# Performance work log

Measured on AMD Instinct MI355X. Metric: run time of the kernel, lower is better.

The kernel has to match this reference:

```python
import jax, jax.numpy as jnp
import numpy as np

N_AGENTS, OBS_DIM, HID, ACT_DIM = 8192, 64, 128, 16


def setup_inputs() -> dict:
    key = jax.random.key(0)
    k = jax.random.split(key, 8)
    obs_agents = jax.random.normal(k[0], (N_AGENTS, OBS_DIM), dtype=jnp.float32)
    # binary adjacency, {0,1}, int32 (index/mask semantics, non-differentiable)
    adj = jax.random.randint(k[1], (N_AGENTS, N_AGENTS), 0, 2, dtype=jnp.int32)
    def lin(kk, fan_in, fan_out):
        lim = 1.0 / np.sqrt(fan_in)
        kw, kb = jax.random.split(kk)
        W = jax.random.uniform(kw, (fan_in, fan_out), jnp.float32, -lim, lim)
        b = jax.random.uniform(kb, (fan_out,), jnp.float32, -lim, lim)
        return W, b
    W1, b1 = lin(k[2], OBS_DIM, HID)          # encoder
    W2, b2 = lin(k[3], 2 * HID, HID)          # actor layer 1
    W3, b3 = lin(k[4], HID, ACT_DIM)          # actor layer 2
    return {"obs_agents": obs_agents, "adj": adj,
            "W1": W1, "b1": b1, "W2": W2, "b2": b2, "W3": W3, "b3": b3}


def reference(obs_agents, adj, W1, b1, W2, b2, W3, b3):
    # per-agent encode: h = tanh(obs @ W1 + b1)  -> [N, HID]
    h = jnp.tanh(obs_agents @ W1 + b1)
    # neighbor mean message: mean of h[j] over j with adj[i,j]!=0, zeros if no neighbors
    a = adj.astype(h.dtype)                      # [N, N] binary
    deg = jnp.sum(a, axis=1, keepdims=True)      # [N, 1]
    msg = (a @ h) / jnp.maximum(deg, 1.0)        # zero rows stay zero
    # actor MLP on concat([h, msg])
    combined = jnp.concatenate([h, msg], axis=-1)            # [N, 2*HID]
    hid = jnp.tanh(combined @ W2 + b2)                        # [N, HID]
    logits = hid @ W3 + b3                                    # [N, ACT_DIM]
    return logits
```

## Files before the change

### kernel.cpp

```cpp
#include <hip/hip_runtime.h>
#include <stdint.h>
#include <math.h>

#define NAG 8192
#define NC  128
#define NSPLIT 8
#define LDB2 136

typedef __attribute__((ext_vector_type(8))) short short8;
typedef __attribute__((ext_vector_type(4))) float floatx4;

__device__ __forceinline__ float bf2f(unsigned short u) {
    union { uint32_t i; float f; } v; v.i = ((uint32_t)u) << 16; return v.f;
}
__device__ __forceinline__ unsigned short f2bf(float f) {
    union { float f; uint32_t i; } v; v.f = f;
    uint32_t x = v.i;
    return (unsigned short)((x + 0x7FFFu + ((x >> 16) & 1u)) >> 16);
}
__device__ __forceinline__ unsigned short f2h(float f) {
    union { _Float16 h; unsigned short u; } v; v.h = (_Float16)f; return v.u;
}
__device__ __forceinline__ float h2f(unsigned short u) {
    union { _Float16 h; unsigned short u; } v; v.u = u; return (float)v.h;
}
__device__ __forceinline__ bool detect_f32(const void* W1, int t) {
    const unsigned short* w = (const unsigned short*)W1;
    int l = t & 63, big = 0;
    #pragma unroll
    for (int j = 0; j < 8; ++j) {
        float v = bf2f(w[l * 8 + j]);
        if (!(fabsf(v) <= 1e6f)) big = 1;
    }
    return __ballot(big) != 0ull;
}

__global__ __launch_bounds__(256) void kE_encode(
    const void* __restrict__ obs,
    const void* __restrict__ W1,
    const void* __restrict__ b1,
    float* __restrict__ h_f32,
    unsigned short* __restrict__ hT)
{
    __shared__ float obs_lds[32][68];
    __shared__ unsigned short ht_lds[128][33];
    const int t = threadIdx.x;
    const int abase = blockIdx.x * 32;
    const bool isf = detect_f32(W1, t);

    {
        int a = t >> 3, c0 = (t & 7) * 8;
        if (isf) {
            const float* p = (const float*)obs;
            #pragma unroll
            for (int j = 0; j < 8; ++j)
                obs_lds[a][c0 + j] = p[(size_t)(abase + a) * 64 + c0 + j];
        } else {
            const unsigned short* p = (const unsigned short*)obs;
            #pragma unroll
            for (int j = 0; j < 8; ++j)
                obs_lds[a][c0 + j] = bf2f(p[(size_t)(abase + a) * 64 + c0 + j]);
        }
    }
    __syncthreads();

    const int o = t & 127;
    const int half = t >> 7;
    float acc[16];
    if (isf) {
        const float* Wp = (const float*)W1;
        float bias = ((const float*)b1)[o];
        #pragma unroll
        for (int i = 0; i < 16; ++i) acc[i] = bias;
        for (int k0 = 0; k0 < 64; k0 += 8) {
            float w[8];
            #pragma unroll
            for (int j = 0; j < 8; ++j) w[j] = Wp[(k0 + j) * 128 + o];
            #pragma unroll
            for (int j = 0; j < 8; ++j)
                #pragma unroll
                for (int i = 0; i < 16; ++i)
                    acc[i] = fmaf(obs_lds[half * 16 + i][k0 + j], w[j], acc[i]);
        }
    } else {
        const unsigned short* Wp = (const unsigned short*)W1;
        float bias = bf2f(((const unsigned short*)b1)[o]);
        #pragma unroll
        for (int i = 0; i < 16; ++i) acc[i] = bias;
        for (int k0 = 0; k0 < 64; k0 += 8) {
            float w[8];
            #pragma unroll
            for (int j = 0; j < 8; ++j) w[j] = bf2f(Wp[(k0 + j) * 128 + o]);
            #pragma unroll
            for (int j = 0; j < 8; ++j)
                #pragma unroll
                for (int i = 0; i < 16; ++i)
                    acc[i] = fmaf(obs_lds[half * 16 + i][k0 + j], w[j], acc[i]);
        }
    }
    #pragma unroll
    for (int i = 0; i < 16; ++i) {
        float th = tanhf(acc[i]);
        int a = half * 16 + i;
        h_f32[(size_t)(abase + a) * 128 + o] = th;
        ht_lds[o][a] = f2bf(th);
    }
    __syncthreads();

    for (int p = 0; p < 16; ++p) {
        int n = p * 8 + (t >> 5);
        int a = t & 31;
        hT[(size_t)n * NAG + abase + a] = ht_lds[n][a];
    }
}

__global__ __launch_bounds__(256, 4) void kG_msggemm(
    const int* __restrict__ adj,
    const unsigned short* __restrict__ hT,
    unsigned short* __restrict__ Cp16,
    int* __restrict__ degP)
{
    __shared__ __align__(16) unsigned short Blds[128 * LDB2];
    const int t = threadIdx.x;
    const int mtile = blockIdx.x & 127;
    const int ks = blockIdx.x >> 7;
    const int row0 = mtile * 64;
    const int kbeg = ks * 1024;

    const int wave = t >> 6, lane = t & 63;
    const int fm = lane & 15, quad = lane >> 4;

    floatx4 acc[8];
    #pragma unroll
    for (int i = 0; i < 8; ++i) acc[i] = (floatx4)0.f;

    const int arow = row0 + wave * 16 + fm;
    const int* ap = adj + (size_t)arow * NAG + kbeg + quad * 8;
    int dsum = 0;

    for (int ss = 0; ss < 8; ++ss) {
        int4 av[8];
        #pragma unroll
        for (int kw = 0; kw < 4; ++kw) {
            av[2 * kw]     = *reinterpret_cast<const int4*>(ap + ss * 128 + kw * 32);
            av[2 * kw + 1] = *reinterpret_cast<const int4*>(ap + ss * 128 + kw * 32 + 4);
        }
        if (ss) __syncthreads();
        #pragma unroll
        for (int i = 0; i < 8; ++i) {
            int idx = i * 256 + t;
            int row = idx >> 4, ch = idx & 15;
            uint4 v = *reinterpret_cast<const uint4*>(hT + (size_t)row * NAG + kbeg + ss * 128 + ch * 8);
            *reinterpret_cast<uint4*>(&Blds[row * LDB2 + ch * 8]) = v;
        }
        __syncthreads();
        #pragma unroll
        for (int kw = 0; kw < 4; ++kw) {
            const int* q = (const int*)&av[2 * kw];
            union { uint32_t u[4]; short8 s; } af;
            #pragma unroll
            for (int p = 0; p < 4; ++p) {
                uint32_t e0 = (q[2 * p]     != 0);
                uint32_t e1 = (q[2 * p + 1] != 0);
                dsum += (int)(e0 + e1);
                af.u[p] = (e0 | (e1 << 16)) * 0x3F80u;
            }
            #pragma unroll
            for (int j = 0; j < 8; ++j) {
                short8 bf = *reinterpret_cast<const short8*>(&Blds[(j * 16 + fm) * LDB2 + kw * 32 + quad * 8]);
                acc[j] = __builtin_amdgcn_mfma_f32_16x16x32_bf16(af.s, bf, acc[j], 0, 0, 0);
            }
        }
    }

    dsum += __shfl_xor(dsum, 16);
    dsum += __shfl_xor(dsum, 32);
    if (lane < 16) degP[ks * NAG + arow] = dsum;

    unsigned short* out = Cp16 + (size_t)ks * (NAG * NC);
    #pragma unroll
    for (int j = 0; j < 8; ++j) {
        int col = j * 16 + fm;
        #pragma unroll
        for (int r = 0; r < 4; ++r) {
            int row = row0 + wave * 16 + quad * 4 + r;
            out[(size_t)row * NC + col] = f2h(acc[j][r]);
        }
    }
}

__global__ __launch_bounds__(256) void k3_actor(
    const float* __restrict__ h_f32,
    const unsigned short* __restrict__ Cp16,
    const int* __restrict__ degP,
    const void* __restrict__ W1,
    const void* __restrict__ W2,
    const void* __restrict__ b2,
    const void* __restrict__ W3,
    const void* __restrict__ b3,
    void* __restrict__ out)
{
    __shared__ float4 comb4[8][66];
    __shared__ float hid[8][132];
    __shared__ int degs[8][9];
    __shared__ float inv_lds[8];
    const int t = threadIdx.x;
    const int abase = blockIdx.x * 8;
    const bool isf = detect_f32(W1, t);
    const size_t PS = (size_t)NAG * NC;

    if (t < 64) {
        int a = t >> 3, s = t & 7;
        degs[a][s] = degP[s * NAG + abase + a];
    }
    __syncthreads();
    if (t < 8) {
        int d = 0;
        #pragma unroll
        for (int s = 0; s < 8; ++s) d += degs[t][s];
        inv_lds[t] = 1.0f / fmaxf((float)d, 1.0f);
    }
    __syncthreads();

    #pragma unroll
    for (int jj = 0; jj < 2; ++jj) {
        int idx = jj * 256 + t;
        int a = idx >> 6, q = idx & 63;
        float4 v;
        if (q < 32) {
            v = *reinterpret_cast<const float4*>(h_f32 + (size_t)(abase + a) * 128 + q * 4);
        } else {
            int f = (q - 32) * 4;
            float s0 = 0.f, s1 = 0.f, s2 = 0.f, s3 = 0.f;
            #pragma unroll
            for (int s = 0; s < NSPLIT; ++s) {
                ushort4 p = *reinterpret_cast<const ushort4*>(Cp16 + s * PS + (size_t)(abase + a) * NC + f);
                s0 += h2f(p.x); s1 += h2f(p.y); s2 += h2f(p.z); s3 += h2f(p.w);
            }
            float sc = inv_lds[a];
            v = make_float4(s0 * sc, s1 * sc, s2 * sc, s3 * sc);
        }
        comb4[a][q] = v;
    }
    __syncthreads();

    const int o = t & 127, half = t >> 7;
    float acc[4];
    if (isf) {
        const float* Wp = (const float*)W2;
        float bias = ((const float*)b2)[o];
        #pragma unroll
        for (int i = 0; i < 4; ++i) acc[i] = bias;
        for (int cq = 0; cq < 64; ++cq) {
            float w0 = Wp[(cq * 4 + 0) * 128 + o];
            float w1 = Wp[(cq * 4 + 1) * 128 + o];
            float w2 = Wp[(cq * 4 + 2) * 128 + o];
            float w3 = Wp[(cq * 4 + 3) * 128 + o];
            #pragma unroll
            for (int i = 0; i < 4; ++i) {
                float4 v = comb4[half * 4 + i][cq];
                acc[i] = fmaf(v.x, w0, acc[i]);
                acc[i] = fmaf(v.y, w1, acc[i]);
                acc[i] = fmaf(v.z, w2, acc[i]);
                acc[i] = fmaf(v.w, w3, acc[i]);
            }
        }
    } else {
        const unsigned short* Wp = (const unsigned short*)W2;
        float bias = bf2f(((const unsigned short*)b2)[o]);
        #pragma unroll
        for (int i = 0; i < 4; ++i) acc[i] = bias;
        for (int cq = 0; cq < 64; ++cq) {
            float w0 = bf2f(Wp[(cq * 4 + 0) * 128 + o]);
            float w1 = bf2f(Wp[(cq * 4 + 1) * 128 + o]);
            float w2 = bf2f(Wp[(cq * 4 + 2) * 128 + o]);
            float w3 = bf2f(Wp[(cq * 4 + 3) * 128 + o]);
            #pragma unroll
            for (int i = 0; i < 4; ++i) {
                float4 v = comb4[half * 4 + i][cq];
                acc[i] = fmaf(v.x, w0, acc[i]);
                acc[i] = fmaf(v.y, w1, acc[i]);
                acc[i] = fmaf(v.z, w2, acc[i]);
                acc[i] = fmaf(v.w, w3, acc[i]);
            }
        }
    }
    #pragma unroll
    for (int i = 0; i < 4; ++i)
        hid[half * 4 + i][o] = tanhf(acc[i]);
    __syncthreads();

    if (t < 128) {
        const int q = t & 15, ar = t >> 4;
        float l;
        if (isf) {
            const float* Wp = (const float*)W3;
            l = ((const float*)b3)[q];
            #pragma unroll 4
            for (int oo = 0; oo < 128; ++oo)
                l = fmaf(hid[ar][oo], Wp[oo * 16 + q], l);
        } else {
            const unsigned short* Wp = (const unsigned short*)W3;
            l = bf2f(((const unsigned short*)b3)[q]);
            #pragma unroll 4
            for (int oo = 0; oo < 128; ++oo)
                l = fmaf(hid[ar][oo], bf2f(Wp[oo * 16 + q]), l);
        }
        size_t i0 = (size_t)(abase + ar) * 16 + q;
        if (isf) ((float*)out)[i0] = l;
        else     ((unsigned short*)out)[i0] = f2bf(l);
    }
}

extern "C" void kernel_launch(void* const* d_in, const int* in_sizes, int n_in,
                              void* d_out, int out_size, void* d_ws, size_t ws_size,
                              hipStream_t stream) {
    const void* obs = d_in[0];
    const int*  adj = (const int*)d_in[1];
    const void* W1  = d_in[2];
    const void* b1  = d_in[3];
    const void* W2  = d_in[4];
    const void* b2  = d_in[5];
    const void* W3  = d_in[6];
    const void* b3  = d_in[7];

    char* ws = (char*)d_ws;
    unsigned short* hT   = (unsigned short*)(ws);
    float*          h_f32= (float*)(ws + 2097152);
    unsigned short* Cp16 = (unsigned short*)(ws + 6291456);
    int*            degP = (int*)(ws + 23068672);

    hipLaunchKernelGGL(kE_encode, dim3(256), dim3(256), 0, stream,
                       obs, W1, b1, h_f32, hT);
    hipLaunchKernelGGL(kG_msggemm, dim3(1024), dim3(256), 0, stream,
                       adj, hT, Cp16, degP);
    hipLaunchKernelGGL(k3_actor, dim3(1024), dim3(256), 0, stream,
                       h_f32, Cp16, degP, W1, W2, b2, W3, b3, d_out);
}
```

Measured before the change: 484.2 us.

## Load adjacency rows coalesced and pack into bitmasks via ballot

The adjacency tile is now read with lanes spanning consecutive columns of one row, so each load is a fully coalesced 256-byte access instead of each lane pulling 32-byte strided chunks from its own row. Each wave ballots the nonzero flags into 64-bit masks, stores them in a small LDS array, and every lane then rebuilds its MFMA A fragment and the degree count from those bits with popcount. This removes the per-element compare work from the fragment path and the degree shuffle reduction. It costs 32 scalar loads per stage instead of 8 vector loads, plus ballot and LDS traffic.

```diff
diff --git a/kernel.cpp b/kernel.cpp
--- a/kernel.cpp
+++ b/kernel.cpp
@@ -121,6 +121,7 @@
     int* __restrict__ degP)
 {
     __shared__ __align__(16) unsigned short Blds[128 * LDB2];
+    __shared__ __align__(16) unsigned long long bitsLds[4][16][2];
     const int t = threadIdx.x;
     const int mtile = blockIdx.x & 127;
     const int ks = blockIdx.x >> 7;
@@ -135,15 +136,15 @@
     for (int i = 0; i < 8; ++i) acc[i] = (floatx4)0.f;
 
     const int arow = row0 + wave * 16 + fm;
-    const int* ap = adj + (size_t)arow * NAG + kbeg + quad * 8;
+    const int* wrows = adj + (size_t)(row0 + wave * 16) * NAG + kbeg;
     int dsum = 0;
 
     for (int ss = 0; ss < 8; ++ss) {
-        int4 av[8];
-        #pragma unroll
-        for (int kw = 0; kw < 4; ++kw) {
-            av[2 * kw]     = *reinterpret_cast<const int4*>(ap + ss * 128 + kw * 32);
-            av[2 * kw + 1] = *reinterpret_cast<const int4*>(ap + ss * 128 + kw * 32 + 4);
+        int va[32];
+        #pragma unroll
+        for (int i = 0; i < 32; ++i) {
+            int r = i >> 1, hh = i & 1;
+            va[i] = wrows[(size_t)r * NAG + ss * 128 + hh * 64 + lane];
         }
         if (ss) __syncthreads();
         #pragma unroll
@@ -153,17 +154,23 @@
             uint4 v = *reinterpret_cast<const uint4*>(hT + (size_t)row * NAG + kbeg + ss * 128 + ch * 8);
             *reinterpret_cast<uint4*>(&Blds[row * LDB2 + ch * 8]) = v;
         }
+        #pragma unroll
+        for (int i = 0; i < 32; ++i) {
+            unsigned long long m = __ballot(va[i] != 0);
+            if (lane == 0) bitsLds[wave][i >> 1][i & 1] = m;
+        }
         __syncthreads();
+        int4 a0 = *reinterpret_cast<const int4*>(&bitsLds[wave][fm][0]);
+        uint32_t aw[4] = {(uint32_t)a0.x, (uint32_t)a0.y, (uint32_t)a0.z, (uint32_t)a0.w};
+        dsum += __popc(aw[0]) + __popc(aw[1]) + __popc(aw[2]) + __popc(aw[3]);
         #pragma unroll
         for (int kw = 0; kw < 4; ++kw) {
-            const int* q = (const int*)&av[2 * kw];
+            uint32_t b = (aw[kw] >> (quad * 8)) & 0xFFu;
             union { uint32_t u[4]; short8 s; } af;
             #pragma unroll
             for (int p = 0; p < 4; ++p) {
-                uint32_t e0 = (q[2 * p]     != 0);
-                uint32_t e1 = (q[2 * p + 1] != 0);
-                dsum += (int)(e0 + e1);
-                af.u[p] = (e0 | (e1 << 16)) * 0x3F80u;
+                uint32_t bb = b >> (2 * p);
+                af.u[p] = ((bb & 1u) | ((bb & 2u) << 15)) * 0x3F80u;
             }
             #pragma unroll
             for (int j = 0; j < 8; ++j) {
@@ -173,9 +180,7 @@
         }
     }
 
-    dsum += __shfl_xor(dsum, 16);
-    dsum += __shfl_xor(dsum, 32);
-    if (lane < 16) degP[ks * NAG + arow] = dsum;
+    if (quad == 0) degP[ks * NAG + arow] = dsum;
 
     unsigned short* out = Cp16 + (size_t)ks * (NAG * NC);
     #pragma unroll
```

Measured after the change: 467.3 us. -3.5%, faster.
